# Kernel optimization log

Hardware: AMD Instinct MI355X
Metric: run time of the kernel (lower is better)

## Reference

```python
import jax, jax.numpy as jnp
import numpy as np

N_NODES = 100000
N_EDGES = 800000
EDGE_NAMES = ["ei_connected_to", "ei_ordered_next", "ei_represents", "ei_represented_by",
              "ei_neighboring_vertical", "ei_neighboring_horizontal", "ei_contains",
              "ei_order", "ei_perpendicular"]
AGGRS_L2 = ["sum", "sum", "mean", "mean", "sum", "sum", "mean"]


def _glorot(key, shape):
    fan_in, fan_out = shape[-2], shape[-1]
    s = (2.0 / (fan_in + fan_out)) ** 0.5
    return jax.random.normal(key, shape, dtype=jnp.float32) * s


def setup_inputs() -> dict:
    key = jax.random.key(0)
    ks = iter(jax.random.split(key, 32))
    inp = {"x": jax.random.normal(next(ks), (N_NODES, 6), dtype=jnp.float32)}
    for name in EDGE_NAMES:
        inp[name] = jax.random.randint(next(ks), (2, N_EDGES), 0, N_NODES, dtype=jnp.int32)
    inp.update(
        W0n=_glorot(next(ks), (2, 6, 16)), W0r=_glorot(next(ks), (2, 6, 16)),
        b0=jnp.zeros((2, 16), jnp.float32),
        W1n=_glorot(next(ks), (2, 16, 32)), W1r=_glorot(next(ks), (2, 16, 32)),
        b1=jnp.zeros((2, 32), jnp.float32),
        P1=_glorot(next(ks), (16, 32)), pb1=jnp.zeros((32,), jnp.float32),
        W2n=_glorot(next(ks), (7, 32, 64)), W2r=_glorot(next(ks), (7, 32, 64)),
        b2=jnp.zeros((7, 64), jnp.float32),
        P2=_glorot(next(ks), (32, 64)), pb2=jnp.zeros((64,), jnp.float32),
    )
    return inp


def _hetero_conv(x, edges, aggrs, Wn, Wr, b):
    # Per-relation GraphConv: out_d = aggr(x[src]->dst) @ Wn_r + x @ Wr_r + b_r,
    # summed across relations (HeteroConv aggr='sum'). Loop is over a small fixed
    # set of relation types (structurally distinct), not data dims.
    n = x.shape[0]
    out = jnp.zeros((n, Wn.shape[-1]), x.dtype)
    for i, (ei, aggr) in enumerate(zip(edges, aggrs)):
        src, dst = ei[0], ei[1]
        msg = jax.ops.segment_sum(x[src], dst, num_segments=n)  # scatter-add gather
        if aggr == "mean":
            cnt = jax.ops.segment_sum(jnp.ones_like(dst, dtype=x.dtype), dst, num_segments=n)
            msg = msg / jnp.maximum(cnt, 1.0)[:, None]
        out = out + msg @ Wn[i] + x @ Wr[i] + b[i]
    return out


def reference(x, W0n, W0r, b0, W1n, W1r, b1, P1, pb1, W2n, W2r, b2, P2, pb2,
              ei_connected_to, ei_ordered_next, ei_represents, ei_represented_by,
              ei_neighboring_vertical, ei_neighboring_horizontal, ei_contains,
              ei_order, ei_perpendicular):
    e01 = [ei_connected_to, ei_ordered_next]
    e2 = [ei_represents, ei_represented_by, ei_neighboring_vertical,
          ei_neighboring_horizontal, ei_contains, ei_order, ei_perpendicular]
    # local head: 6 -> 16 (two sum relations)
    h = _hetero_conv(x, e01, ["sum", "sum"], W0n, W0r, b0)
    # residual block 1: 16 -> 32 (same two sum relations, linear residual projection)
    h = jax.nn.relu(_hetero_conv(h, e01, ["sum", "sum"], W1n, W1r, b1) + h @ P1 + pb1)
    # residual block 2: 32 -> 64 (seven relations, sum/mean aggregation)
    h = jax.nn.relu(_hetero_conv(h, e2, AGGRS_L2, W2n, W2r, b2) + h @ P2 + pb2)
    # final elementwise relu from SemanticModule.forward
    return jax.nn.relu(h)
```

## Files before the change

### kernel.cpp

```cpp
#include <hip/hip_runtime.h>

#define NN 100000
#define NE 800000
#define NRG 128
#define SPAN 784
#define CAP 8192
#define NBIN (9 * NRG)

typedef _Float16 f16;
typedef __attribute__((ext_vector_type(4))) _Float16 f16x4;
typedef __attribute__((ext_vector_type(8))) _Float16 f16x8;
typedef __attribute__((ext_vector_type(4))) float f32x4;
typedef __attribute__((ext_vector_type(2))) float f32x2;

struct EPtrs { const int* s[9]; const int* d[9]; };

__global__ __launch_bounds__(256) void prep_weights(
    const float* __restrict__ W0n, const float* __restrict__ W0r, const float* __restrict__ b0,
    const float* __restrict__ W1n, const float* __restrict__ W1r, const float* __restrict__ b1,
    const float* __restrict__ P1,  const float* __restrict__ pb1,
    const float* __restrict__ W2n, const float* __restrict__ W2r, const float* __restrict__ b2,
    const float* __restrict__ P2,  const float* __restrict__ pb2,
    float* __restrict__ wc0, float* __restrict__ bc0,
    float* __restrict__ wc1, float* __restrict__ bc1,
    f16*   __restrict__ b2frag, float* __restrict__ bc2,
    int*   __restrict__ cursor)
{
    int tid = threadIdx.x;
    for (int t = tid; t < NBIN; t += 256) cursor[t] = 0;

    for (int t = tid; t < 18 * 16; t += 256) {
        int row = t >> 4, col = t & 15;
        float v;
        if (row < 6)       v = W0n[row * 16 + col];
        else if (row < 12) v = W0n[96 + (row - 6) * 16 + col];
        else               v = W0r[(row - 12) * 16 + col] + W0r[96 + (row - 12) * 16 + col];
        wc0[t] = v;
    }
    for (int t = tid; t < 16; t += 256) bc0[t] = b0[t] + b0[16 + t];

    for (int t = tid; t < 48 * 32; t += 256) {
        int row = t >> 5, col = t & 31;
        float v;
        if (row < 16)      v = W1n[row * 32 + col];
        else if (row < 32) v = W1n[512 + (row - 16) * 32 + col];
        else { int rr = row - 32; v = W1r[rr * 32 + col] + W1r[512 + rr * 32 + col] + P1[rr * 32 + col]; }
        wc1[t] = v;
    }
    for (int t = tid; t < 32; t += 256) bc1[t] = b1[t] + b1[32 + t] + pb1[t];

    for (int t = tid; t < 256 * 64; t += 256) {
        int j = t & 7, lane = (t >> 3) & 63, ntk = t >> 9;
        int nt = ntk & 3, kt = ntk >> 2;
        int k = kt * 32 + (lane >> 4) * 8 + j;
        int n = nt * 16 + (lane & 15);
        float v;
        if (k < 224) v = W2n[k * 64 + n];
        else {
            int rr = k - 224;
            v = P2[rr * 64 + n];
            #pragma unroll
            for (int r = 0; r < 7; ++r) v += W2r[r * 2048 + rr * 64 + n];
        }
        b2frag[t] = (f16)v;
    }
    for (int t = tid; t < 64; t += 256) {
        float v = pb2[t];
        #pragma unroll
        for (int r = 0; r < 7; ++r) v += b2[r * 64 + t];
        bc2[t] = v;
    }
}

__global__ __launch_bounds__(256) void passA(EPtrs ep, int* __restrict__ cursor,
                                             unsigned* __restrict__ binbuf)
{
    int r = blockIdx.y;
    int e0 = blockIdx.x * 4096;
    int cnt = min(4096, NE - e0);
    int tid = threadIdx.x;
    __shared__ int h[NRG];
    __shared__ int bs[NRG + 1];
    __shared__ int cl[NRG];
    __shared__ int gb[NRG];
    __shared__ int auxtot;
    __shared__ unsigned pk[4096];

    if (tid < NRG) h[tid] = 0;
    __syncthreads();

    const int* dp = ep.d[r];
    const int* sp = ep.s[r];
    unsigned wv[16];
    int rgk[16];
    #pragma unroll
    for (int k = 0; k < 16; ++k) {
        int e = e0 + k * 256 + tid;
        rgk[k] = -1;
        if (e < NE) {
            int d = dp[e];
            int sv = sp[e];
            int g = d / SPAN;
            int l = d - g * SPAN;
            wv[k] = ((unsigned)l << 17) | (unsigned)sv;
            rgk[k] = g;
            atomicAdd(&h[g], 1);
        }
    }
    __syncthreads();

    int vcnt = 0, incl = 0;
    if (tid < NRG) {
        vcnt = h[tid];
        incl = vcnt;
        int lane = tid & 63;
        #pragma unroll
        for (int ofs = 1; ofs < 64; ofs <<= 1) {
            int u = __shfl_up(incl, ofs, 64);
            if (lane >= ofs) incl += u;
        }
        if (tid == 63) auxtot = incl;
    }
    __syncthreads();
    if (tid < NRG) {
        int excl = incl - vcnt + ((tid >= 64) ? auxtot : 0);
        bs[tid] = excl;
        cl[tid] = excl;
        gb[tid] = (vcnt > 0) ? atomicAdd(&cursor[r * NRG + tid], vcnt) : 0;
        if (tid == NRG - 1) bs[NRG] = excl + vcnt;
    }
    __syncthreads();

    #pragma unroll
    for (int k = 0; k < 16; ++k) {
        if (rgk[k] >= 0) {
            int p = atomicAdd(&cl[rgk[k]], 1);
            pk[p] = wv[k];
        }
    }
    __syncthreads();

    for (int i = tid; i < cnt; i += 256) {
        int loB = 0, hiB = NRG;
        while (hiB - loB > 1) {
            int mid = (loB + hiB) >> 1;
            if (bs[mid] <= i) loB = mid; else hiB = mid;
        }
        int b = loB;
        int pos = gb[b] + (i - bs[b]);
        if (pos < CAP)
            binbuf[((size_t)(r * NRG + b)) * CAP + pos] = pk[i];
    }
}

__global__ __launch_bounds__(256) void passB(const unsigned* __restrict__ binbuf,
                                             const int* __restrict__ cursor,
                                             int* __restrict__ deg, int* __restrict__ off,
                                             int* __restrict__ eidx)
{
    int bin = blockIdx.x;
    int r = bin >> 7, rg = bin & (NRG - 1);
    int lo = rg * SPAN;
    int n_here = min(SPAN, NN - lo);
    int tid = threadIdx.x;
    __shared__ int h[SPAN];
    __shared__ int wsum[4];
    __shared__ int stage[CAP];

    int sz = min(cursor[bin], CAP);
    const unsigned* bp = binbuf + (size_t)bin * CAP;

    for (int i = tid; i < SPAN; i += 256) h[i] = 0;
    __syncthreads();
    for (int e = tid; e < sz; e += 256) atomicAdd(&h[bp[e] >> 17], 1);
    __syncthreads();

    int i0 = tid * 4;
    int dstash[4];
    int s = 0;
    #pragma unroll
    for (int k = 0; k < 4; ++k) {
        int i = i0 + k;
        int v = (i < SPAN) ? h[i] : 0;
        dstash[k] = v;
        s += v;
    }
    int lane = tid & 63, wid = tid >> 6;
    int incl = s;
    #pragma unroll
    for (int ofs = 1; ofs < 64; ofs <<= 1) {
        int u = __shfl_up(incl, ofs, 64);
        if (lane >= ofs) incl += u;
    }
    if (lane == 63) wsum[wid] = incl;
    __syncthreads();
    if (tid == 0) {
        int a = wsum[0], b = wsum[1], c = wsum[2];
        wsum[0] = 0; wsum[1] = a; wsum[2] = a + b; wsum[3] = a + b + c;
    }
    __syncthreads();
    int run = incl - s + wsum[wid];
    int base = bin * CAP;
    #pragma unroll
    for (int k = 0; k < 4; ++k) {
        int i = i0 + k;
        if (i < SPAN) {
            int v = dstash[k];
            h[i] = run;
            if (i < n_here) {
                deg[r * NN + lo + i] = v;
                off[r * NN + lo + i] = base + run + v;
            }
            run += v;
        }
    }
    __syncthreads();

    for (int e = tid; e < sz; e += 256) {
        unsigned w = bp[e];
        int p = atomicAdd(&h[w >> 17], 1);
        stage[p] = (int)(w & 0x1FFFF);
    }
    __syncthreads();
    for (int i = tid; i < sz; i += 256) eidx[base + i] = stage[i];
}

__global__ __launch_bounds__(256, 2) void t0f(const float* __restrict__ x,
                                              const int* __restrict__ deg, const int* __restrict__ off,
                                              const int* __restrict__ eidx,
                                              const float* __restrict__ wc0, const float* __restrict__ bc0,
                                              f16* __restrict__ h0h)
{
    __shared__ float sw[288 + 16];
    for (int t = threadIdx.x; t < 304; t += 256) sw[t] = (t < 288) ? wc0[t] : bc0[t - 288];
    __syncthreads();
    int n = blockIdx.x * 256 + threadIdx.x;
    if (n >= NN) return;
    float acc[16];
    #pragma unroll
    for (int j = 0; j < 16; ++j) acc[j] = sw[288 + j];
    float xv[6];
    {
        const float2* xp = reinterpret_cast<const float2*>(x + (size_t)n * 6);
        float2 a = xp[0], b = xp[1], c = xp[2];
        xv[0] = a.x; xv[1] = a.y; xv[2] = b.x; xv[3] = b.y; xv[4] = c.x; xv[5] = c.y;
    }
    #pragma unroll
    for (int r = 0; r < 2; ++r) {
        float m[6] = {0, 0, 0, 0, 0, 0};
        int e1 = off[r * NN + n];
        int e0 = e1 - deg[r * NN + n];
        int e = e0;
        for (; e + 2 <= e1; e += 2) {
            int sA = eidx[e], sB = eidx[e + 1];
            const float2* pA = reinterpret_cast<const float2*>(x + (size_t)sA * 6);
            const float2* pB = reinterpret_cast<const float2*>(x + (size_t)sB * 6);
            float2 a0 = pA[0], a1 = pA[1], a2 = pA[2];
            float2 b0 = pB[0], b1 = pB[1], b2 = pB[2];
            m[0] += a0.x + b0.x; m[1] += a0.y + b0.y;
            m[2] += a1.x + b1.x; m[3] += a1.y + b1.y;
            m[4] += a2.x + b2.x; m[5] += a2.y + b2.y;
        }
        if (e < e1) {
            int sA = eidx[e];
            const float2* pA = reinterpret_cast<const float2*>(x + (size_t)sA * 6);
            float2 a0 = pA[0], a1 = pA[1], a2 = pA[2];
            m[0] += a0.x; m[1] += a0.y; m[2] += a1.x; m[3] += a1.y; m[4] += a2.x; m[5] += a2.y;
        }
        #pragma unroll
        for (int k = 0; k < 6; ++k) {
            float s = m[k];
            #pragma unroll
            for (int j = 0; j < 16; ++j) acc[j] = fmaf(s, sw[(r * 6 + k) * 16 + j], acc[j]);
        }
    }
    #pragma unroll
    for (int k = 0; k < 6; ++k) {
        float s = xv[k];
        #pragma unroll
        for (int j = 0; j < 16; ++j) acc[j] = fmaf(s, sw[(12 + k) * 16 + j], acc[j]);
    }
    f16x8 o0, o1;
    #pragma unroll
    for (int j = 0; j < 8; ++j) { o0[j] = (f16)acc[j]; o1[j] = (f16)acc[8 + j]; }
    f16x8* op = reinterpret_cast<f16x8*>(h0h + (size_t)n * 16);
    op[0] = o0; op[1] = o1;
}

__global__ __launch_bounds__(256) void g1(const int* __restrict__ deg, const int* __restrict__ off,
                                          const int* __restrict__ eidx, const f16* __restrict__ h0h,
                                          f16* __restrict__ msum)
{
    int t = blockIdx.x * 256 + threadIdx.x;
    int node = t >> 2, l = t & 3;
    if (node >= NN) return;
    int dd[2], oo[2];
    #pragma unroll
    for (int r = 0; r < 2; ++r) { dd[r] = deg[r * NN + node]; oo[r] = off[r * NN + node]; }
    #pragma unroll 1
    for (int r = 0; r < 2; ++r) {
        int e1 = oo[r];
        int e0 = e1 - dd[r];
        float a0 = 0.f, a1 = 0.f, a2 = 0.f, a3 = 0.f;
        int e = e0;
        for (; e + 4 <= e1; e += 4) {
            int sA = eidx[e], sB = eidx[e + 1], sC = eidx[e + 2], sD = eidx[e + 3];
            f16x4 vA = *reinterpret_cast<const f16x4*>(h0h + (size_t)sA * 16 + l * 4);
            f16x4 vB = *reinterpret_cast<const f16x4*>(h0h + (size_t)sB * 16 + l * 4);
            f16x4 vC = *reinterpret_cast<const f16x4*>(h0h + (size_t)sC * 16 + l * 4);
            f16x4 vD = *reinterpret_cast<const f16x4*>(h0h + (size_t)sD * 16 + l * 4);
            a0 += (float)vA[0] + (float)vB[0] + (float)vC[0] + (float)vD[0];
            a1 += (float)vA[1] + (float)vB[1] + (float)vC[1] + (float)vD[1];
            a2 += (float)vA[2] + (float)vB[2] + (float)vC[2] + (float)vD[2];
            a3 += (float)vA[3] + (float)vB[3] + (float)vC[3] + (float)vD[3];
        }
        for (; e < e1; ++e) {
            f16x4 v = *reinterpret_cast<const f16x4*>(h0h + (size_t)eidx[e] * 16 + l * 4);
            a0 += (float)v[0]; a1 += (float)v[1]; a2 += (float)v[2]; a3 += (float)v[3];
        }
        f16x4 o;
        o[0] = (f16)a0; o[1] = (f16)a1; o[2] = (f16)a2; o[3] = (f16)a3;
        *reinterpret_cast<f16x4*>(msum + (size_t)node * 32 + r * 16 + l * 4) = o;
    }
}

__global__ __launch_bounds__(256) void t1t(const f16* __restrict__ h0h, const f16* __restrict__ msum,
                                           const float* __restrict__ wc1, const float* __restrict__ bc1,
                                           f16* __restrict__ h1h, unsigned* __restrict__ h1q)
{
    __shared__ float sw[1536 + 32];
    for (int t = threadIdx.x; t < 1568; t += 256) sw[t] = (t < 1536) ? wc1[t] : bc1[t - 1536];
    __syncthreads();
    int n = blockIdx.x * 256 + threadIdx.x;
    if (n >= NN) return;
    float acc[32];
    #pragma unroll
    for (int j = 0; j < 32; ++j) acc[j] = sw[1536 + j];
    {
        const f16x8* mp = reinterpret_cast<const f16x8*>(msum + (size_t)n * 32);
        f16x8 m0 = mp[0], m1 = mp[1], m2 = mp[2], m3 = mp[3];
        #pragma unroll
        for (int k = 0; k < 8; ++k) {
            float s0 = (float)m0[k], s1 = (float)m1[k];
            float s2 = (float)m2[k], s3 = (float)m3[k];
            #pragma unroll
            for (int j = 0; j < 32; ++j)
                acc[j] += s0 * sw[k * 32 + j] + s1 * sw[(8 + k) * 32 + j]
                        + s2 * sw[(16 + k) * 32 + j] + s3 * sw[(24 + k) * 32 + j];
        }
    }
    {
        const f16x8* hp = reinterpret_cast<const f16x8*>(h0h + (size_t)n * 16);
        f16x8 a = hp[0], b = hp[1];
        #pragma unroll
        for (int k = 0; k < 8; ++k) {
            float s0 = (float)a[k], s1 = (float)b[k];
            #pragma unroll
            for (int j = 0; j < 32; ++j)
                acc[j] = fmaf(s0, sw[(32 + k) * 32 + j], fmaf(s1, sw[(40 + k) * 32 + j], acc[j]));
        }
    }
    #pragma unroll
    for (int j = 0; j < 32; ++j) acc[j] = fmaxf(acc[j], 0.f);

    f16x8* op = reinterpret_cast<f16x8*>(h1h + (size_t)n * 32);
    #pragma unroll
    for (int q = 0; q < 4; ++q) {
        f16x8 o;
        #pragma unroll
        for (int j = 0; j < 8; ++j) o[j] = (f16)acc[q * 8 + j];
        op[q] = o;
    }
    unsigned qw[8];
    #pragma unroll
    for (int q = 0; q < 8; ++q) {
        int w = __builtin_amdgcn_cvt_pk_fp8_f32(acc[q * 4 + 0], acc[q * 4 + 1], 0, false);
        w = __builtin_amdgcn_cvt_pk_fp8_f32(acc[q * 4 + 2], acc[q * 4 + 3], w, true);
        qw[q] = (unsigned)w;
    }
    uint4* qp = reinterpret_cast<uint4*>(h1q + (size_t)n * 8);
    qp[0] = make_uint4(qw[0], qw[1], qw[2], qw[3]);
    qp[1] = make_uint4(qw[4], qw[5], qw[6], qw[7]);
}

__global__ __launch_bounds__(256, 8) void g2t2(const int* __restrict__ deg, const int* __restrict__ off,
                                               const int* __restrict__ eidx, const unsigned* __restrict__ h1q,
                                               const f16* __restrict__ h1h, const f16* __restrict__ b2frag,
                                               const float* __restrict__ bc2, float* __restrict__ out)
{
    __shared__ f16 cat[16][264];

    int tid = threadIdx.x;
    int nloc = tid >> 4;
    int half = (tid >> 3) & 1;
    int l = tid & 7;
    int node = blockIdx.x * 16 + nloc;

    if (half == 0) {
        f16x4 v = *reinterpret_cast<const f16x4*>(h1h + (size_t)node * 32 + l * 4);
        *reinterpret_cast<f16x4*>(&cat[nloc][224 + l * 4]) = v;
    }

    int dd[4], oo[4];
    #pragma unroll
    for (int rr = 0; rr < 4; ++rr) {
        int r = half * 4 + rr;
        bool ok = (r < 7);
        dd[rr] = ok ? deg[(r + 2) * NN + node] : 0;
        oo[rr] = ok ? off[(r + 2) * NN + node] : 0;
    }

    #pragma unroll 1
    for (int rr = 0; rr < 4; ++rr) {
        int r = half * 4 + rr;
        if (r >= 7) break;
        int e1 = oo[rr];
        int e0 = e1 - dd[rr];
        float a0 = 0.f, a1 = 0.f, a2 = 0.f, a3 = 0.f;
        int e = e0;
        for (; e + 4 <= e1; e += 4) {
            int sA = eidx[e], sB = eidx[e + 1], sC = eidx[e + 2], sD = eidx[e + 3];
            unsigned wA = h1q[(size_t)sA * 8 + l];
            unsigned wB = h1q[(size_t)sB * 8 + l];
            unsigned wC = h1q[(size_t)sC * 8 + l];
            unsigned wD = h1q[(size_t)sD * 8 + l];
            f32x2 lA = __builtin_amdgcn_cvt_pk_f32_fp8(wA, false), hA = __builtin_amdgcn_cvt_pk_f32_fp8(wA, true);
            f32x2 lB = __builtin_amdgcn_cvt_pk_f32_fp8(wB, false), hB = __builtin_amdgcn_cvt_pk_f32_fp8(wB, true);
            f32x2 lC = __builtin_amdgcn_cvt_pk_f32_fp8(wC, false), hC = __builtin_amdgcn_cvt_pk_f32_fp8(wC, true);
            f32x2 lD = __builtin_amdgcn_cvt_pk_f32_fp8(wD, false), hD = __builtin_amdgcn_cvt_pk_f32_fp8(wD, true);
            a0 += lA[0] + lB[0] + lC[0] + lD[0];
            a1 += lA[1] + lB[1] + lC[1] + lD[1];
            a2 += hA[0] + hB[0] + hC[0] + hD[0];
            a3 += hA[1] + hB[1] + hC[1] + hD[1];
        }
        for (; e < e1; ++e) {
            unsigned w = h1q[(size_t)eidx[e] * 8 + l];
            f32x2 lo = __builtin_amdgcn_cvt_pk_f32_fp8(w, false);
            f32x2 hi = __builtin_amdgcn_cvt_pk_f32_fp8(w, true);
            a0 += lo[0]; a1 += lo[1]; a2 += hi[0]; a3 += hi[1];
        }
        float sc = (r == 2 || r == 3 || r == 6) ? (1.0f / (float)max(dd[rr], 1)) : 1.0f;
        f16x4 o;
        o[0] = (f16)(a0 * sc); o[1] = (f16)(a1 * sc); o[2] = (f16)(a2 * sc); o[3] = (f16)(a3 * sc);
        *reinterpret_cast<f16x4*>(&cat[nloc][r * 32 + l * 4]) = o;
    }

    int lane = tid & 63, w = tid >> 6;
    int quad = lane >> 4, col0 = lane & 15;
    float bcv = bc2[w * 16 + col0];

    __syncthreads();

    f32x4 acc = (f32x4){0.f, 0.f, 0.f, 0.f};
    #pragma unroll
    for (int kt = 0; kt < 8; ++kt) {
        f16x8 a = *reinterpret_cast<const f16x8*>(&cat[col0][kt * 32 + quad * 8]);
        f16x8 b = *reinterpret_cast<const f16x8*>(b2frag + ((size_t)(kt * 4 + w) * 64 + lane) * 8);
        acc = __builtin_amdgcn_mfma_f32_16x16x32_f16(a, b, acc, 0, 0, 0);
    }

    int row0 = blockIdx.x * 16 + quad * 4;
    #pragma unroll
    for (int i = 0; i < 4; ++i)
        out[(size_t)(row0 + i) * 64 + w * 16 + col0] = fmaxf(acc[i] + bcv, 0.f);
}

extern "C" void kernel_launch(void* const* d_in, const int* in_sizes, int n_in,
                              void* d_out, int out_size, void* d_ws, size_t ws_size,
                              hipStream_t stream)
{
    const float* x = (const float*)d_in[0];
    EPtrs ep;
    for (int i = 0; i < 9; ++i) { const int* p = (const int*)d_in[1 + i]; ep.s[i] = p; ep.d[i] = p + NE; }
    const float* W0n = (const float*)d_in[10]; const float* W0r = (const float*)d_in[11];
    const float* b0  = (const float*)d_in[12];
    const float* W1n = (const float*)d_in[13]; const float* W1r = (const float*)d_in[14];
    const float* b1  = (const float*)d_in[15];
    const float* P1  = (const float*)d_in[16]; const float* pb1 = (const float*)d_in[17];
    const float* W2n = (const float*)d_in[18]; const float* W2r = (const float*)d_in[19];
    const float* b2  = (const float*)d_in[20];
    const float* P2  = (const float*)d_in[21]; const float* pb2 = (const float*)d_in[22];
    float* out = (float*)d_out;
    char* ws = (char*)d_ws;

    size_t off_b = 0;
    auto alloc = [&](size_t b) { size_t o = off_b; off_b += (b + 255) & ~(size_t)255; return o; };
    size_t o_wc0 = alloc(288 * 4);   size_t o_bc0 = alloc(16 * 4);
    size_t o_wc1 = alloc(1536 * 4);  size_t o_bc1 = alloc(32 * 4);
    size_t o_b2f = alloc(16384 * 2); size_t o_bc2 = alloc(64 * 4);
    size_t o_h0h = alloc((size_t)NN * 16 * 2);
    size_t o_h1q = alloc((size_t)NN * 32);
    size_t o_msum = alloc((size_t)NN * 32 * 2);
    size_t o_h1h = alloc((size_t)NN * 32 * 2);
    size_t o_bin = alloc((size_t)NBIN * CAP * 4);
    size_t o_deg = alloc((size_t)9 * NN * 4);
    size_t o_off = alloc((size_t)9 * NN * 4);
    size_t o_eid = alloc((size_t)NBIN * CAP * 4);
    size_t o_cur = alloc((size_t)NBIN * 4);
    (void)ws_size;

    float* wc0 = (float*)(ws + o_wc0); float* bc0 = (float*)(ws + o_bc0);
    float* wc1 = (float*)(ws + o_wc1); float* bc1 = (float*)(ws + o_bc1);
    f16*   b2f = (f16*)(ws + o_b2f);   float* bc2 = (float*)(ws + o_bc2);
    f16*   h0h = (f16*)(ws + o_h0h);
    unsigned* h1q = (unsigned*)(ws + o_h1q);
    f16*   msum = (f16*)(ws + o_msum);
    f16*   h1h = (f16*)(ws + o_h1h);
    unsigned* binbuf = (unsigned*)(ws + o_bin);
    int*   deg = (int*)(ws + o_deg);
    int*   offp = (int*)(ws + o_off);
    int*   eid = (int*)(ws + o_eid);
    int*   cur = (int*)(ws + o_cur);

    dim3 B(256);
    prep_weights<<<1, B, 0, stream>>>(W0n, W0r, b0, W1n, W1r, b1, P1, pb1,
                                      W2n, W2r, b2, P2, pb2,
                                      wc0, bc0, wc1, bc1, b2f, bc2, cur);
    passA<<<dim3((NE + 4095) / 4096, 9), B, 0, stream>>>(ep, cur, binbuf);
    passB<<<NBIN, B, 0, stream>>>(binbuf, cur, deg, offp, eid);

    t0f<<<(NN + 255) / 256, B, 0, stream>>>(x, deg, offp, eid, wc0, bc0, h0h);
    g1<<<(NN * 4 + 255) / 256, B, 0, stream>>>(deg, offp, eid, h0h, msum);
    t1t<<<(NN + 255) / 256, B, 0, stream>>>(h0h, msum, wc1, bc1, h1h, h1q);
    g2t2<<<NN / 16, B, 0, stream>>>(deg, offp, eid, h1q, h1h, b2f, bc2, out);
}
```

Measured before the change: 332.6 us.

## Remap layer-2 gather so each lane handles one relation half with 16-byte loads

The layer-2 gather kernel now gives each pair of lanes one relation, with each lane loading a 16-byte half-row of the fp8 feature table per edge, instead of 8 lanes each loading 4 bytes while walking four relations in sequence. All seven relations are processed in parallel within a node group, and the two spare lanes copy the self features. The B-fragment weight loads are hoisted ahead of the barrier so they overlap the gather. The change cuts the number of memory transactions and serial relation loops, but uses more registers per lane and spreads per-lane work unevenly across relations with different degrees.

```diff
diff --git a/kernel.cpp b/kernel.cpp
--- a/kernel.cpp
+++ b/kernel.cpp
@@ -392,71 +392,91 @@
 
     int tid = threadIdx.x;
     int nloc = tid >> 4;
-    int half = (tid >> 3) & 1;
-    int l = tid & 7;
+    int lane16 = tid & 15;
     int node = blockIdx.x * 16 + nloc;
 
-    if (half == 0) {
-        f16x4 v = *reinterpret_cast<const f16x4*>(h1h + (size_t)node * 32 + l * 4);
-        *reinterpret_cast<f16x4*>(&cat[nloc][224 + l * 4]) = v;
-    }
-
-    int dd[4], oo[4];
-    #pragma unroll
-    for (int rr = 0; rr < 4; ++rr) {
-        int r = half * 4 + rr;
-        bool ok = (r < 7);
-        dd[rr] = ok ? deg[(r + 2) * NN + node] : 0;
-        oo[rr] = ok ? off[(r + 2) * NN + node] : 0;
-    }
-
-    #pragma unroll 1
-    for (int rr = 0; rr < 4; ++rr) {
-        int r = half * 4 + rr;
-        if (r >= 7) break;
-        int e1 = oo[rr];
-        int e0 = e1 - dd[rr];
-        float a0 = 0.f, a1 = 0.f, a2 = 0.f, a3 = 0.f;
+    if (lane16 >= 14) {
+        int part = lane16 - 14;
+        const f16x8* hp = reinterpret_cast<const f16x8*>(h1h + (size_t)node * 32 + part * 16);
+        f16x8 v0 = hp[0], v1 = hp[1];
+        *reinterpret_cast<f16x8*>(&cat[nloc][224 + part * 16]) = v0;
+        *reinterpret_cast<f16x8*>(&cat[nloc][224 + part * 16 + 8]) = v1;
+    } else {
+        int r = lane16 >> 1;
+        int half = lane16 & 1;
+        int d = deg[(r + 2) * NN + node];
+        int e1 = off[(r + 2) * NN + node];
+        int e0 = e1 - d;
+
+        f32x2 acc[8];
+        #pragma unroll
+        for (int q = 0; q < 8; ++q) acc[q] = (f32x2){0.f, 0.f};
+
+        const uint4* tbl = reinterpret_cast<const uint4*>(h1q);
         int e = e0;
-        for (; e + 4 <= e1; e += 4) {
-            int sA = eidx[e], sB = eidx[e + 1], sC = eidx[e + 2], sD = eidx[e + 3];
-            unsigned wA = h1q[(size_t)sA * 8 + l];
-            unsigned wB = h1q[(size_t)sB * 8 + l];
-            unsigned wC = h1q[(size_t)sC * 8 + l];
-            unsigned wD = h1q[(size_t)sD * 8 + l];
-            f32x2 lA = __builtin_amdgcn_cvt_pk_f32_fp8(wA, false), hA = __builtin_amdgcn_cvt_pk_f32_fp8(wA, true);
-            f32x2 lB = __builtin_amdgcn_cvt_pk_f32_fp8(wB, false), hB = __builtin_amdgcn_cvt_pk_f32_fp8(wB, true);
-            f32x2 lC = __builtin_amdgcn_cvt_pk_f32_fp8(wC, false), hC = __builtin_amdgcn_cvt_pk_f32_fp8(wC, true);
-            f32x2 lD = __builtin_amdgcn_cvt_pk_f32_fp8(wD, false), hD = __builtin_amdgcn_cvt_pk_f32_fp8(wD, true);
-            a0 += lA[0] + lB[0] + lC[0] + lD[0];
-            a1 += lA[1] + lB[1] + lC[1] + lD[1];
-            a2 += hA[0] + hB[0] + hC[0] + hD[0];
-            a3 += hA[1] + hB[1] + hC[1] + hD[1];
-        }
-        for (; e < e1; ++e) {
-            unsigned w = h1q[(size_t)eidx[e] * 8 + l];
-            f32x2 lo = __builtin_amdgcn_cvt_pk_f32_fp8(w, false);
-            f32x2 hi = __builtin_amdgcn_cvt_pk_f32_fp8(w, true);
-            a0 += lo[0]; a1 += lo[1]; a2 += hi[0]; a3 += hi[1];
-        }
-        float sc = (r == 2 || r == 3 || r == 6) ? (1.0f / (float)max(dd[rr], 1)) : 1.0f;
-        f16x4 o;
-        o[0] = (f16)(a0 * sc); o[1] = (f16)(a1 * sc); o[2] = (f16)(a2 * sc); o[3] = (f16)(a3 * sc);
-        *reinterpret_cast<f16x4*>(&cat[nloc][r * 32 + l * 4]) = o;
+        for (; e + 2 <= e1; e += 2) {
+            int sA = eidx[e], sB = eidx[e + 1];
+            uint4 qA = tbl[(size_t)sA * 2 + half];
+            uint4 qB = tbl[(size_t)sB * 2 + half];
+            acc[0] += __builtin_amdgcn_cvt_pk_f32_fp8(qA.x, false);
+            acc[1] += __builtin_amdgcn_cvt_pk_f32_fp8(qA.x, true);
+            acc[2] += __builtin_amdgcn_cvt_pk_f32_fp8(qA.y, false);
+            acc[3] += __builtin_amdgcn_cvt_pk_f32_fp8(qA.y, true);
+            acc[4] += __builtin_amdgcn_cvt_pk_f32_fp8(qA.z, false);
+            acc[5] += __builtin_amdgcn_cvt_pk_f32_fp8(qA.z, true);
+            acc[6] += __builtin_amdgcn_cvt_pk_f32_fp8(qA.w, false);
+            acc[7] += __builtin_amdgcn_cvt_pk_f32_fp8(qA.w, true);
+            acc[0] += __builtin_amdgcn_cvt_pk_f32_fp8(qB.x, false);
+            acc[1] += __builtin_amdgcn_cvt_pk_f32_fp8(qB.x, true);
+            acc[2] += __builtin_amdgcn_cvt_pk_f32_fp8(qB.y, false);
+            acc[3] += __builtin_amdgcn_cvt_pk_f32_fp8(qB.y, true);
+            acc[4] += __builtin_amdgcn_cvt_pk_f32_fp8(qB.z, false);
+            acc[5] += __builtin_amdgcn_cvt_pk_f32_fp8(qB.z, true);
+            acc[6] += __builtin_amdgcn_cvt_pk_f32_fp8(qB.w, false);
+            acc[7] += __builtin_amdgcn_cvt_pk_f32_fp8(qB.w, true);
+        }
+        if (e < e1) {
+            int sA = eidx[e];
+            uint4 qA = tbl[(size_t)sA * 2 + half];
+            acc[0] += __builtin_amdgcn_cvt_pk_f32_fp8(qA.x, false);
+            acc[1] += __builtin_amdgcn_cvt_pk_f32_fp8(qA.x, true);
+            acc[2] += __builtin_amdgcn_cvt_pk_f32_fp8(qA.y, false);
+            acc[3] += __builtin_amdgcn_cvt_pk_f32_fp8(qA.y, true);
+            acc[4] += __builtin_amdgcn_cvt_pk_f32_fp8(qA.z, false);
+            acc[5] += __builtin_amdgcn_cvt_pk_f32_fp8(qA.z, true);
+            acc[6] += __builtin_amdgcn_cvt_pk_f32_fp8(qA.w, false);
+            acc[7] += __builtin_amdgcn_cvt_pk_f32_fp8(qA.w, true);
+        }
+
+        float sc = (r == 2 || r == 3 || r == 6) ? (1.0f / (float)max(d, 1)) : 1.0f;
+        f16x8 o0, o1;
+        #pragma unroll
+        for (int q = 0; q < 4; ++q) {
+            o0[q * 2 + 0] = (f16)(acc[q][0] * sc);
+            o0[q * 2 + 1] = (f16)(acc[q][1] * sc);
+            o1[q * 2 + 0] = (f16)(acc[4 + q][0] * sc);
+            o1[q * 2 + 1] = (f16)(acc[4 + q][1] * sc);
+        }
+        *reinterpret_cast<f16x8*>(&cat[nloc][r * 32 + half * 16]) = o0;
+        *reinterpret_cast<f16x8*>(&cat[nloc][r * 32 + half * 16 + 8]) = o1;
     }
 
     int lane = tid & 63, w = tid >> 6;
     int quad = lane >> 4, col0 = lane & 15;
     float bcv = bc2[w * 16 + col0];
 
+    f16x8 bfr[8];
+    #pragma unroll
+    for (int kt = 0; kt < 8; ++kt)
+        bfr[kt] = *reinterpret_cast<const f16x8*>(b2frag + ((size_t)(kt * 4 + w) * 64 + lane) * 8);
+
     __syncthreads();
 
     f32x4 acc = (f32x4){0.f, 0.f, 0.f, 0.f};
     #pragma unroll
     for (int kt = 0; kt < 8; ++kt) {
         f16x8 a = *reinterpret_cast<const f16x8*>(&cat[col0][kt * 32 + quad * 8]);
-        f16x8 b = *reinterpret_cast<const f16x8*>(b2frag + ((size_t)(kt * 4 + w) * 64 + lane) * 8);
-        acc = __builtin_amdgcn_mfma_f32_16x16x32_f16(a, b, acc, 0, 0, 0);
+        acc = __builtin_amdgcn_mfma_f32_16x16x32_f16(a, bfr[kt], acc, 0, 0, 0);
     }
 
     int row0 = blockIdx.x * 16 + quad * 4;
```

Result: no change. 326.6 us (-1.8%).
